# Kernel tuning notes

Hardware: AMD Instinct MI355X
Metric: run time of the kernel (lower is better)

The kernel has to match this reference:

```python
import jax, jax.numpy as jnp
import numpy as np

B, L, H = 32, 4096, 64
C_U, C_X, N_OUT = 3, 1, 1
NL = 4
MODES = [512, 1024, 2048]


def setup_inputs() -> dict:
    key = jax.random.key(0)
    ks = jax.random.split(key, 16)
    scale = 1.0 / H  # 1/sqrt(in_ch*out_ch) with in_ch=out_ch=H
    inp = {
        'u': jax.random.normal(ks[0], (B, C_U, L), dtype=jnp.float32),
        'x': jax.random.uniform(ks[1], (B, C_X, L), dtype=jnp.float32),
        'enc_w': jax.random.normal(ks[2], (H, C_U + C_X), dtype=jnp.float32) * 0.5,
        'enc_b': jax.random.normal(ks[3], (H,), dtype=jnp.float32) * 0.1,
        'dec_w': jax.random.normal(ks[4], (N_OUT, H), dtype=jnp.float32) * 0.125,
        'dec_b': jax.random.normal(ks[5], (N_OUT,), dtype=jnp.float32) * 0.1,
        'conv1_w': jax.random.normal(ks[6], (NL, H, H), dtype=jnp.float32) * 0.125,
        'conv1_b': jax.random.normal(ks[7], (NL, H), dtype=jnp.float32) * 0.1,
        'conv2_w': jax.random.normal(ks[8], (NL, H, H), dtype=jnp.float32) * 0.125,
        'conv2_b': jax.random.normal(ks[9], (NL, H), dtype=jnp.float32) * 0.1,
        'spec_w0': jax.random.normal(ks[10], (NL, H, H, MODES[0], 2), dtype=jnp.float32) * scale,
        'spec_b0': jax.random.normal(ks[11], (NL, H), dtype=jnp.float32) * 0.1,
        'spec_w1': jax.random.normal(ks[12], (NL, H, H, MODES[1], 2), dtype=jnp.float32) * scale,
        'spec_b1': jax.random.normal(ks[13], (NL, H), dtype=jnp.float32) * 0.1,
        'spec_w2': jax.random.normal(ks[14], (NL, H, H, MODES[2], 2), dtype=jnp.float32) * scale,
        'spec_b2': jax.random.normal(ks[15], (NL, H), dtype=jnp.float32) * 0.1,
    }
    return inp


def _conv1x1(w, b, v):
    # 1x1 Conv1d: (O,I) x (B,I,L) -> (B,O,L)
    return jnp.einsum('oi,bil->bol', w, v) + b[None, :, None]


def _spectral(v, w_ri, b, n):
    # w_ri: (I,O,m,2) real/imag; v: (B,I,L)
    w = w_ri[..., 0] + 1j * w_ri[..., 1]
    m = w.shape[-1]
    x_low = jnp.fft.rfft(v, axis=-1)[:, :, :m]          # (B,I,m) complex
    y_ft = jnp.einsum('bim,iom->bom', x_low, w)          # (B,O,m)
    y = jnp.fft.irfft(y_ft, n=n, axis=-1)                # (B,O,L) real
    return y + b[None, :, None]


def reference(u, x, enc_w, enc_b, dec_w, dec_b, conv1_w, conv1_b, conv2_w, conv2_b,
              spec_w0, spec_b0, spec_w1, spec_b1, spec_w2, spec_b2):
    v = jnp.concatenate([x, u], axis=1)                  # (B, C_X+C_U, L)
    v = _conv1x1(enc_w, enc_b, v)                        # (B, H, L)
    spec_ws = (spec_w0, spec_w1, spec_w2)
    spec_bs = (spec_b0, spec_b1, spec_b2)
    n = v.shape[-1]
    for l in range(NL):
        spec_sum = _spectral(v, spec_ws[0][l], spec_bs[0][l], n)
        for k in range(1, len(spec_ws)):
            spec_sum = spec_sum + _spectral(v, spec_ws[k][l], spec_bs[k][l], n)
        h = jax.nn.gelu(_conv1x1(conv1_w[l], conv1_b[l], spec_sum))
        v = v + _conv1x1(conv2_w[l], conv2_b[l], h)
    return _conv1x1(dec_w, dec_b, v)                     # (B, N_OUT, L)
```

## Files before the change

### kernel.cpp

```cpp
#include <hip/hip_runtime.h>
#include <math.h>

#ifndef M_PI
#define M_PI 3.14159265358979323846
#endif

#define LEN   4096
#define NB    32
#define NH    64
#define NF    2048
#define NLAYER 4

__device__ __forceinline__ float2 cmul(float2 a, float2 b) {
    return make_float2(a.x*b.x - a.y*b.y, a.x*b.y + a.y*b.x);
}

__device__ __forceinline__ void twpow16(float2 w1, float2 W[16]) {
    W[0] = make_float2(1.0f, 0.0f);
    W[1] = w1;
    W[2] = cmul(w1, w1);
    W[3] = cmul(W[2], W[1]);
    W[4] = cmul(W[2], W[2]);
    W[5] = cmul(W[4], W[1]);
    W[6] = cmul(W[4], W[2]);
    W[7] = cmul(W[4], W[3]);
    W[8] = cmul(W[4], W[4]);
    W[9]  = cmul(W[8], W[1]);
    W[10] = cmul(W[8], W[2]);
    W[11] = cmul(W[8], W[3]);
    W[12] = cmul(W[8], W[4]);
    W[13] = cmul(W[8], W[5]);
    W[14] = cmul(W[8], W[6]);
    W[15] = cmul(W[8], W[7]);
}

__device__ __forceinline__ void gll16(const void* g, void* l) {
    __builtin_amdgcn_global_load_lds(
        (const __attribute__((address_space(1))) void*)g,
        (__attribute__((address_space(3))) void*)l, 16, 0, 0);
}

__global__ __launch_bounds__(256) void fill_tw(float2* __restrict__ tw) {
    int k = blockIdx.x * 256 + threadIdx.x;
    if (k < 4096) {
        double ang = -2.0 * M_PI * (double)k / 4096.0;
        tw[k] = make_float2((float)cos(ang), (float)sin(ang));
    }
}

__global__ __launch_bounds__(256) void w2t_k(
        const float* __restrict__ w2, float* __restrict__ w2t) {
    int idx = blockIdx.x * 256 + threadIdx.x;
    int l = idx >> 12;
    int r = idx & 4095;
    int o = r >> 6, i = r & 63;
    w2t[l * 4096 + i * 64 + o] = w2[idx];
}

#define BR16_INIT const int BR[16] = {0,8,4,12,2,10,6,14,1,9,5,13,3,11,7,15}

template<bool INV>
__device__ __forceinline__ void fft16(float2 z[16]) {
    const float S  = INV ? 1.0f : -1.0f;
    const float C1 = 0.9238795325112867f, S1 = 0.3826834323650898f;
    const float C2 = 0.7071067811865476f;
    const float2 W16[8] = {{1.f,0.f},{C1,S*S1},{C2,S*C2},{S1,S*C1},
                           {0.f,S},{-S1,S*C1},{-C2,S*C2},{-C1,S*S1}};
    const float2 W8[4]  = {{1.f,0.f},{C2,S*C2},{0.f,S},{-C2,S*C2}};
    #pragma unroll
    for (int i = 0; i < 8; ++i) {
        float2 u = z[i], v = z[i+8];
        z[i]   = make_float2(u.x+v.x, u.y+v.y);
        float2 d = make_float2(u.x-v.x, u.y-v.y);
        z[i+8] = cmul(d, W16[i]);
    }
    #pragma unroll
    for (int h = 0; h < 16; h += 8)
        #pragma unroll
        for (int i = 0; i < 4; ++i) {
            float2 u = z[h+i], v = z[h+i+4];
            z[h+i]   = make_float2(u.x+v.x, u.y+v.y);
            float2 d = make_float2(u.x-v.x, u.y-v.y);
            z[h+i+4] = cmul(d, W8[i]);
        }
    #pragma unroll
    for (int h = 0; h < 16; h += 4) {
        { float2 u = z[h],   v = z[h+2];
          z[h]   = make_float2(u.x+v.x, u.y+v.y);
          z[h+2] = make_float2(u.x-v.x, u.y-v.y); }
        { float2 u = z[h+1], v = z[h+3];
          z[h+1] = make_float2(u.x+v.x, u.y+v.y);
          float2 d = make_float2(u.x-v.x, u.y-v.y);
          z[h+3] = make_float2(-S*d.y, S*d.x); }
    }
    #pragma unroll
    for (int h = 0; h < 16; h += 2) {
        float2 u = z[h], v = z[h+1];
        z[h]   = make_float2(u.x+v.x, u.y+v.y);
        z[h+1] = make_float2(u.x-v.x, u.y-v.y);
    }
}

__global__ __launch_bounds__(256) void encoder_k(
        const float* __restrict__ x, const float* __restrict__ u,
        const float* __restrict__ ew, const float* __restrict__ eb,
        float* __restrict__ v) {
    int tid = blockIdx.x * 256 + threadIdx.x;
    int b = tid >> 12;
    int l = tid & (LEN - 1);
    float xv = x[(size_t)b * LEN + l];
    float u0 = u[((size_t)b * 3 + 0) * LEN + l];
    float u1 = u[((size_t)b * 3 + 1) * LEN + l];
    float u2 = u[((size_t)b * 3 + 2) * LEN + l];
    for (int h = 0; h < NH; ++h) {
        float a = eb[h] + ew[h*4+0]*xv + ew[h*4+1]*u0 + ew[h*4+2]*u1 + ew[h*4+3]*u2;
        v[((size_t)b * NH + h) * LEN + l] = a;
    }
}

__global__ __launch_bounds__(256) void fft_fwd_k(
        const float* __restrict__ vin, float2* __restrict__ Xt,
        const float2* __restrict__ tw) {
    __shared__ float2 lds[4352];
    BR16_INIT;
    int p = blockIdx.x;
    const float* s1 = vin + (size_t)(2*p)   * LEN;
    const float* s2 = vin + (size_t)(2*p+1) * LEN;
    int t = threadIdx.x;
    float2 z[16];
    #pragma unroll
    for (int a = 0; a < 16; ++a)
        z[a] = make_float2(s1[a*256 + t], s2[a*256 + t]);
    fft16<false>(z);
    {
        float2 Wp[16];
        twpow16(tw[t], Wp);
        #pragma unroll
        for (int r = 0; r < 16; ++r) {
            int ka = BR[r];
            lds[ka*256 + t] = cmul(z[r], Wp[ka]);
        }
    }
    __syncthreads();
    int ka = t >> 4, bp = t & 15;
    #pragma unroll
    for (int a2 = 0; a2 < 16; ++a2)
        z[a2] = lds[ka*256 + a2*16 + bp];
    __syncthreads();
    fft16<false>(z);
    {
        float2 Wq[16];
        twpow16(tw[16*bp], Wq);
        #pragma unroll
        for (int r = 0; r < 16; ++r) {
            int kap = BR[r];
            lds[kap*272 + ka*17 + bp] = cmul(z[r], Wq[kap]);
        }
    }
    __syncthreads();
    int kap2 = t >> 4, ka2 = t & 15;
    #pragma unroll
    for (int b2 = 0; b2 < 16; ++b2)
        z[b2] = lds[kap2*272 + ka2*17 + b2];
    __syncthreads();
    fft16<false>(z);
    #pragma unroll
    for (int r = 0; r < 16; ++r)
        lds[t + 256*BR[r]] = z[r];
    __syncthreads();
    float2* d1 = Xt + (size_t)(2*p)   * NF;
    float2* d2 = Xt + (size_t)(2*p+1) * NF;
    for (int j = 0; j < 8; ++j) {
        int f = t + j * 256;
        float2 Zf = lds[f];
        float2 Zm = lds[(4096 - f) & 4095];
        d1[f] = make_float2(0.5f * (Zf.x + Zm.x), 0.5f * (Zf.y - Zm.y));
        d2[f] = make_float2(0.5f * (Zf.y + Zm.y), 0.5f * (Zm.x - Zf.x));
    }
}

__global__ __launch_bounds__(256) void fft_inv_k(
        const float2* __restrict__ Yt, float* __restrict__ sout,
        const float2* __restrict__ tw,
        const float* __restrict__ sb0, const float* __restrict__ sb1,
        const float* __restrict__ sb2, int layer) {
    __shared__ float2 lds[4352];
    BR16_INIT;
    int p = blockIdx.x;
    int o = (2 * p) & (NH - 1);
    const float2* s1 = Yt + (size_t)(2*p)   * NF;
    const float2* s2 = Yt + (size_t)(2*p+1) * NF;
    int t = threadIdx.x;
    float2 z[16];
    #pragma unroll
    for (int a = 0; a < 16; ++a) {
        int f = a * 256 + t;
        float2 zf;
        if (f < 2048) {
            float2 y1 = s1[f];
            float2 y2 = s2[f];
            if (f == 0) zf = make_float2(y1.x, y2.x);
            else        zf = make_float2(y1.x - y2.y, y1.y + y2.x);
        } else if (f == 2048) {
            zf = make_float2(0.0f, 0.0f);
        } else {
            int m = 4096 - f;
            float2 y1 = s1[m];
            float2 y2 = s2[m];
            zf = make_float2(y1.x + y2.y, y2.x - y1.y);
        }
        z[a] = zf;
    }
    fft16<true>(z);
    {
        float2 w1 = tw[t]; w1.y = -w1.y;
        float2 Wp[16];
        twpow16(w1, Wp);
        #pragma unroll
        for (int r = 0; r < 16; ++r) {
            int ka = BR[r];
            lds[ka*256 + t] = cmul(z[r], Wp[ka]);
        }
    }
    __syncthreads();
    int ka = t >> 4, bp = t & 15;
    #pragma unroll
    for (int a2 = 0; a2 < 16; ++a2)
        z[a2] = lds[ka*256 + a2*16 + bp];
    __syncthreads();
    fft16<true>(z);
    {
        float2 w16 = tw[16*bp]; w16.y = -w16.y;
        float2 Wq[16];
        twpow16(w16, Wq);
        #pragma unroll
        for (int r = 0; r < 16; ++r) {
            int kap = BR[r];
            lds[kap*272 + ka*17 + bp] = cmul(z[r], Wq[kap]);
        }
    }
    __syncthreads();
    int kap2 = t >> 4, ka2 = t & 15;
    #pragma unroll
    for (int b2 = 0; b2 < 16; ++b2)
        z[b2] = lds[kap2*272 + ka2*17 + b2];
    fft16<true>(z);
    float bias1 = sb0[layer*NH+o]   + sb1[layer*NH+o]   + sb2[layer*NH+o];
    float bias2 = sb0[layer*NH+o+1] + sb1[layer*NH+o+1] + sb2[layer*NH+o+1];
    float* d1 = sout + (size_t)(2*p)   * LEN;
    float* d2 = sout + (size_t)(2*p+1) * LEN;
    const float sc = 1.0f / 4096.0f;
    #pragma unroll
    for (int r = 0; r < 16; ++r) {
        int l = t + 256 * BR[r];
        d1[l] = z[r].x * sc + bias1;
        d2[l] = z[r].y * sc + bias2;
    }
}

__global__ __launch_bounds__(256) void specmm_k(
        const float2* __restrict__ X, float2* __restrict__ Y,
        const float* __restrict__ w0, const float* __restrict__ w1,
        const float* __restrict__ w2, int layer) {
    __shared__ float2 Xb[2][1024];
    __shared__ float2 Wb[2][512];

    int n   = blockIdx.x;
    int xcd = n & 7;
    int s   = n >> 3;
    int og  = s & 3;
    int tl  = s >> 2;
    int ftile = (tl & 3) * 64 + (tl >> 2) * 8 + xcd;
    int f0 = ftile * 8;
    const bool has1 = (f0 < 1024);
    const bool has0 = (f0 < 512);

    const float2* w2b = (const float2*)w2 + (size_t)layer * NH * NH * 2048;
    const float2* w1b = (const float2*)w1 + (size_t)layer * NH * NH * 1024;
    const float2* w0b = (const float2*)w0 + (size_t)layer * NH * NH * 512;

    int t  = threadIdx.x;
    int ff = t & 7;
    int u  = t >> 3;
    int b0  = (u & 7) * 4;
    int oo0 = (u >> 3) * 4;

    const int wv = t >> 6;
    const int ln = t & 63;
    const int bs = ln >> 2;
    const int sl = ln & 3;

    float2 acc[4][4];
    #pragma unroll
    for (int bb = 0; bb < 4; ++bb)
        #pragma unroll
        for (int oo = 0; oo < 4; ++oo)
            acc[bb][oo] = make_float2(0.0f, 0.0f);

    const float2* gx0; const float2* gx1;
    {
        int b = bs;
        int fp = sl ^ ((b >> 2) & 3);
        gx0 = X + ((size_t)b * NH + wv) * 2048 + f0 + 2*fp;
        b = 16 + bs;
        fp = sl ^ ((b >> 2) & 3);
        gx1 = X + ((size_t)b * NH + wv) * 2048 + f0 + 2*fp;
    }
    const size_t io = (size_t)wv * NH + og * 16 + bs;
    const float2* gw2 = w2b + io * 2048 + f0 + 2*sl;
    const float2* gw1 = w1b + io * 1024 + f0 + 2*sl;
    const float2* gw0 = w0b + io * 512  + f0 + 2*sl;

    #define STAGE_X(ic_, nb_)                                                   \
    {                                                                           \
        gll16(gx0 + (size_t)(ic_)*4*2048, &Xb[nb_][(wv*32 +  0)*8]);            \
        gll16(gx1 + (size_t)(ic_)*4*2048, &Xb[nb_][(wv*32 + 16)*8]);            \
    }
    float2 l2a, l2b, l1a, l1b, l0a, l0b;
    #define WISSUE(ic_)                                                         \
    {                                                                           \
        const float2* p2 = gw2 + (size_t)(ic_)*256*2048;                        \
        l2a = p2[0]; l2b = p2[1];                                               \
        if (has1) { const float2* p1 = gw1 + (size_t)(ic_)*256*1024;            \
                    l1a = p1[0]; l1b = p1[1]; }                                 \
        if (has0) { const float2* p0 = gw0 + (size_t)(ic_)*256*512;             \
                    l0a = p0[0]; l0b = p0[1]; }                                 \
    }
    #define WSUM_STORE(nb_)                                                     \
    {                                                                           \
        float2 wa = l2a, wc = l2b;                                              \
        if (has1) { wa.x += l1a.x; wa.y += l1a.y; wc.x += l1b.x; wc.y += l1b.y; } \
        if (has0) { wa.x += l0a.x; wa.y += l0a.y; wc.x += l0b.x; wc.y += l0b.y; } \
        Wb[nb_][wv*128 + ln*2]     = wa;                                        \
        Wb[nb_][wv*128 + ln*2 + 1] = wc;                                        \
    }

    WISSUE(0);
    STAGE_X(0, 0);
    WSUM_STORE(0);
    __syncthreads();
    int buf = 0;
    for (int ic = 0; ic < 16; ++ic) {
        if (ic < 15) { STAGE_X(ic + 1, buf ^ 1); WISSUE(ic + 1); }
        #pragma unroll
        for (int ii = 0; ii < 4; ++ii) {
            float2 xr[4], wr[4];
            #pragma unroll
            for (int bb = 0; bb < 4; ++bb) {
                int b = b0 + bb;
                int slot = (ff >> 1) ^ ((b >> 2) & 3);
                xr[bb] = Xb[buf][((ii*32 + b)*4 + slot)*2 + (ff & 1)];
            }
            #pragma unroll
            for (int oo = 0; oo < 4; ++oo)
                wr[oo] = Wb[buf][((ii*16 + oo0 + oo)*4 + (ff >> 1))*2 + (ff & 1)];
            #pragma unroll
            for (int bb = 0; bb < 4; ++bb)
                #pragma unroll
                for (int oo = 0; oo < 4; ++oo) {
                    acc[bb][oo].x += xr[bb].x * wr[oo].x - xr[bb].y * wr[oo].y;
                    acc[bb][oo].y += xr[bb].x * wr[oo].y + xr[bb].y * wr[oo].x;
                }
        }
        if (ic < 15) WSUM_STORE(buf ^ 1);
        __syncthreads();
        buf ^= 1;
    }
    #undef STAGE_X
    #undef WISSUE
    #undef WSUM_STORE

    #pragma unroll
    for (int bb = 0; bb < 4; ++bb)
        #pragma unroll
        for (int oo = 0; oo < 4; ++oo)
            Y[((size_t)(b0 + bb) * NH + og * 16 + oo0 + oo) * 2048 + f0 + ff] = acc[bb][oo];
}

__global__ __launch_bounds__(256) void conv_fused_k(
        const float* __restrict__ s,
        const float* __restrict__ c1w, const float* __restrict__ c1b,
        const float* __restrict__ w2t, const float* __restrict__ c2b,
        int layer, float* __restrict__ v,
        const float* __restrict__ dw, const float* __restrict__ db,
        float* __restrict__ out, int last) {
    int tid = blockIdx.x * 256 + threadIdx.x;
    int b = tid >> 12;
    int l = tid & (LEN - 1);
    float xr[NH];
    #pragma unroll
    for (int i = 0; i < NH; ++i) xr[i] = s[((size_t)b * NH + i) * LEN + l];
    const float* w1 = c1w + (size_t)layer * NH * NH;
    const float* b1 = c1b + layer * NH;
    const float* w2 = w2t + (size_t)layer * NH * NH;
    const float* b2 = c2b + layer * NH;
    float acc2[NH];
    #pragma unroll
    for (int o = 0; o < NH; ++o) acc2[o] = b2[o];
    for (int i = 0; i < NH; ++i) {
        const float* wr = w1 + i * NH;
        float a0 = 0.0f, a1 = 0.0f, a2 = 0.0f, a3 = 0.0f;
        #pragma unroll
        for (int k = 0; k < NH; k += 4) {
            a0 += wr[k]     * xr[k];
            a1 += wr[k + 1] * xr[k + 1];
            a2 += wr[k + 2] * xr[k + 2];
            a3 += wr[k + 3] * xr[k + 3];
        }
        float acc = b1[i] + ((a0 + a1) + (a2 + a3));
        float cc = 0.7978845608028654f * (acc + 0.044715f * acc * acc * acc);
        float e  = __expf(2.0f * cc);
        float th = 1.0f - 2.0f / (e + 1.0f);
        float h  = 0.5f * acc * (1.0f + th);
        const float* wc = w2 + i * NH;
        #pragma unroll
        for (int o = 0; o < NH; ++o) acc2[o] += wc[o] * h;
    }
    if (!last) {
        #pragma unroll
        for (int o = 0; o < NH; ++o) {
            size_t idx = ((size_t)b * NH + o) * LEN + l;
            v[idx] = v[idx] + acc2[o];
        }
    } else {
        float acc = db[0];
        #pragma unroll
        for (int o = 0; o < NH; ++o) {
            size_t idx = ((size_t)b * NH + o) * LEN + l;
            acc += dw[o] * (v[idx] + acc2[o]);
        }
        out[(size_t)b * LEN + l] = acc;
    }
}

extern "C" void kernel_launch(void* const* d_in, const int* in_sizes, int n_in,
                              void* d_out, int out_size, void* d_ws, size_t ws_size,
                              hipStream_t stream) {
    const float* u_in   = (const float*)d_in[0];
    const float* x_in   = (const float*)d_in[1];
    const float* enc_w  = (const float*)d_in[2];
    const float* enc_b  = (const float*)d_in[3];
    const float* dec_w  = (const float*)d_in[4];
    const float* dec_b  = (const float*)d_in[5];
    const float* conv1w = (const float*)d_in[6];
    const float* conv1b = (const float*)d_in[7];
    const float* conv2w = (const float*)d_in[8];
    const float* conv2b = (const float*)d_in[9];
    const float* sw0    = (const float*)d_in[10];
    const float* sb0    = (const float*)d_in[11];
    const float* sw1    = (const float*)d_in[12];
    const float* sb1    = (const float*)d_in[13];
    const float* sw2    = (const float*)d_in[14];
    const float* sb2    = (const float*)d_in[15];

    const size_t CPLX = (size_t)2048 * 2048;
    const size_t REAL = (size_t)NB * NH * LEN;
    char* base = (char*)d_ws;
    float2* tw   = (float2*)base;
    float2* bufA = (float2*)(base + 32768);
    float2* bufB = bufA + CPLX;
    float*  sbuf = (float*)(bufB + CPLX);
    float*  vbuf = sbuf + REAL;
    float*  w2tb = vbuf + REAL;
    size_t need = 32768 + 2 * CPLX * sizeof(float2) + 2 * REAL * sizeof(float)
                + (size_t)NLAYER * NH * NH * sizeof(float);
    if (ws_size < need) return;

    fill_tw<<<16, 256, 0, stream>>>(tw);
    w2t_k<<<64, 256, 0, stream>>>(conv2w, w2tb);
    encoder_k<<<(NB * LEN) / 256, 256, 0, stream>>>(x_in, u_in, enc_w, enc_b, vbuf);

    for (int l = 0; l < NLAYER; ++l) {
        fft_fwd_k  <<<NB * NH / 2, 256, 0, stream>>>(vbuf, bufA, tw);
        specmm_k   <<<1024, 256, 0, stream>>>(bufA, bufB, sw0, sw1, sw2, l);
        fft_inv_k  <<<NB * NH / 2, 256, 0, stream>>>(bufB, sbuf, tw,
                                                     sb0, sb1, sb2, l);
        conv_fused_k<<<(NB * LEN) / 256, 256, 0, stream>>>(sbuf, conv1w, conv1b,
                                                           w2tb, conv2b, l, vbuf,
                                                           dec_w, dec_b, (float*)d_out,
                                                           l == NLAYER - 1);
    }
}
```

Measured before the change: 1.149 ms.

## Tile fused conv1x1-GELU-conv1x1 through shared memory with 4x4 register blocking

The fused pointwise-conv kernel used to give each thread one sequence position, holding 64 inputs and 64 accumulators in registers. It now loads a 64-channel by 64-position tile into LDS and has each thread compute a 4x4 output block for both matmuls, with the GELU intermediate staged in a second LDS tile. The final-layer decoder reduction goes through a shared-memory partial sum. This cuts register pressure and gives better weight reuse, at the cost of two barriers and more LDS traffic per block.

```diff
diff --git a/kernel.cpp b/kernel.cpp
--- a/kernel.cpp
+++ b/kernel.cpp
@@ -384,52 +384,114 @@
         int layer, float* __restrict__ v,
         const float* __restrict__ dw, const float* __restrict__ db,
         float* __restrict__ out, int last) {
-    int tid = blockIdx.x * 256 + threadIdx.x;
-    int b = tid >> 12;
-    int l = tid & (LEN - 1);
-    float xr[NH];
-    #pragma unroll
-    for (int i = 0; i < NH; ++i) xr[i] = s[((size_t)b * NH + i) * LEN + l];
+    __shared__ float Ss[64][65];
+    __shared__ float Hs[64][65];
+    int blk = blockIdx.x;
+    int b  = blk >> 6;
+    int l0 = (blk & 63) * 64;
+    int t  = threadIdx.x;
+
+    const float* sb = s + (size_t)b * NH * LEN + l0;
+    #pragma unroll
+    for (int j = 0; j < 16; ++j) {
+        int e = t + 256 * j;
+        Ss[e >> 6][e & 63] = sb[(size_t)(e >> 6) * LEN + (e & 63)];
+    }
+    __syncthreads();
+
     const float* w1 = c1w + (size_t)layer * NH * NH;
     const float* b1 = c1b + layer * NH;
+    int ti = t >> 4;
+    int tl = t & 15;
+
+    {
+        float acc[4][4];
+        #pragma unroll
+        for (int di = 0; di < 4; ++di) {
+            float bias = b1[ti*4 + di];
+            #pragma unroll
+            for (int dl = 0; dl < 4; ++dl) acc[di][dl] = bias;
+        }
+        for (int k4 = 0; k4 < 64; k4 += 4) {
+            float sv[4][4];
+            #pragma unroll
+            for (int kk = 0; kk < 4; ++kk)
+                #pragma unroll
+                for (int dl = 0; dl < 4; ++dl)
+                    sv[kk][dl] = Ss[k4 + kk][tl + 16*dl];
+            #pragma unroll
+            for (int di = 0; di < 4; ++di) {
+                float4 wv = *(const float4*)&w1[(ti*4 + di)*64 + k4];
+                #pragma unroll
+                for (int dl = 0; dl < 4; ++dl)
+                    acc[di][dl] += wv.x*sv[0][dl] + wv.y*sv[1][dl]
+                                 + wv.z*sv[2][dl] + wv.w*sv[3][dl];
+            }
+        }
+        #pragma unroll
+        for (int di = 0; di < 4; ++di)
+            #pragma unroll
+            for (int dl = 0; dl < 4; ++dl) {
+                float a  = acc[di][dl];
+                float cc = 0.7978845608028654f * (a + 0.044715f * a * a * a);
+                float e  = __expf(2.0f * cc);
+                float th = 1.0f - 2.0f / (e + 1.0f);
+                Hs[ti*4 + di][tl + 16*dl] = 0.5f * a * (1.0f + th);
+            }
+    }
+    __syncthreads();
+
     const float* w2 = w2t + (size_t)layer * NH * NH;
     const float* b2 = c2b + layer * NH;
-    float acc2[NH];
-    #pragma unroll
-    for (int o = 0; o < NH; ++o) acc2[o] = b2[o];
-    for (int i = 0; i < NH; ++i) {
-        const float* wr = w1 + i * NH;
-        float a0 = 0.0f, a1 = 0.0f, a2 = 0.0f, a3 = 0.0f;
-        #pragma unroll
-        for (int k = 0; k < NH; k += 4) {
-            a0 += wr[k]     * xr[k];
-            a1 += wr[k + 1] * xr[k + 1];
-            a2 += wr[k + 2] * xr[k + 2];
-            a3 += wr[k + 3] * xr[k + 3];
-        }
-        float acc = b1[i] + ((a0 + a1) + (a2 + a3));
-        float cc = 0.7978845608028654f * (acc + 0.044715f * acc * acc * acc);
-        float e  = __expf(2.0f * cc);
-        float th = 1.0f - 2.0f / (e + 1.0f);
-        float h  = 0.5f * acc * (1.0f + th);
-        const float* wc = w2 + i * NH;
-        #pragma unroll
-        for (int o = 0; o < NH; ++o) acc2[o] += wc[o] * h;
-    }
+    float acc2[4][4];
+    #pragma unroll
+    for (int dq = 0; dq < 4; ++dq) {
+        float bias = b2[ti*4 + dq];
+        #pragma unroll
+        for (int dl = 0; dl < 4; ++dl) acc2[dq][dl] = bias;
+    }
+    for (int i = 0; i < 64; ++i) {
+        float hv[4];
+        #pragma unroll
+        for (int dl = 0; dl < 4; ++dl) hv[dl] = Hs[i][tl + 16*dl];
+        #pragma unroll
+        for (int dq = 0; dq < 4; ++dq) {
+            float wv = w2[i*64 + ti*4 + dq];
+            #pragma unroll
+            for (int dl = 0; dl < 4; ++dl) acc2[dq][dl] += wv * hv[dl];
+        }
+    }
+
     if (!last) {
         #pragma unroll
-        for (int o = 0; o < NH; ++o) {
-            size_t idx = ((size_t)b * NH + o) * LEN + l;
-            v[idx] = v[idx] + acc2[o];
-        }
+        for (int dq = 0; dq < 4; ++dq)
+            #pragma unroll
+            for (int dl = 0; dl < 4; ++dl) {
+                size_t idx = ((size_t)b * NH + ti*4 + dq) * LEN + l0 + tl + 16*dl;
+                v[idx] = v[idx] + acc2[dq][dl];
+            }
     } else {
-        float acc = db[0];
-        #pragma unroll
-        for (int o = 0; o < NH; ++o) {
-            size_t idx = ((size_t)b * NH + o) * LEN + l;
-            acc += dw[o] * (v[idx] + acc2[o]);
-        }
-        out[(size_t)b * LEN + l] = acc;
+        float part[4];
+        #pragma unroll
+        for (int dl = 0; dl < 4; ++dl) part[dl] = 0.0f;
+        #pragma unroll
+        for (int dq = 0; dq < 4; ++dq) {
+            float w = dw[ti*4 + dq];
+            #pragma unroll
+            for (int dl = 0; dl < 4; ++dl) {
+                size_t idx = ((size_t)b * NH + ti*4 + dq) * LEN + l0 + tl + 16*dl;
+                part[dl] += w * (v[idx] + acc2[dq][dl]);
+            }
+        }
+        #pragma unroll
+        for (int dl = 0; dl < 4; ++dl) Ss[tl + 16*dl][ti] = part[dl];
+        __syncthreads();
+        if (t < 64) {
+            float acc = db[0];
+            #pragma unroll
+            for (int g = 0; g < 16; ++g) acc += Ss[t][g];
+            out[(size_t)b * LEN + l0 + t] = acc;
+        }
     }
 }
 
@@ -475,9 +537,9 @@
         specmm_k   <<<1024, 256, 0, stream>>>(bufA, bufB, sw0, sw1, sw2, l);
         fft_inv_k  <<<NB * NH / 2, 256, 0, stream>>>(bufB, sbuf, tw,
                                                      sb0, sb1, sb2, l);
-        conv_fused_k<<<(NB * LEN) / 256, 256, 0, stream>>>(sbuf, conv1w, conv1b,
-                                                           w2tb, conv2b, l, vbuf,
-                                                           dec_w, dec_b, (float*)d_out,
-                                                           l == NLAYER - 1);
-    }
-}
+        conv_fused_k<<<NB * 64, 256, 0, stream>>>(sbuf, conv1w, conv1b,
+                                                  w2tb, conv2b, l, vbuf,
+                                                  dec_w, dec_b, (float*)d_out,
+                                                  l == NLAYER - 1);
+    }
+}
```

Result: faster. 1.073 ms, median of 2 (-6.7%).
